# Kernel optimization log

Measured on AMD Instinct MI355X. Metric: run time of the kernel, lower is better.

The kernel has to match this reference:

```python
import jax, jax.numpy as jnp
import numpy as np

EPS = 1e-5

def _layer_norm_last(x):
    # F.layer_norm over the last dim, no affine
    m = jnp.mean(x, axis=-1, keepdims=True)
    v = jnp.var(x, axis=-1, keepdims=True)
    return (x - m) * jax.lax.rsqrt(v + EPS)

def setup_inputs() -> dict:
    key = jax.random.key(0)
    ks = jax.random.split(key, 4)
    N, C, H, W = 8, 512, 32, 32
    G = 8
    x = jax.random.normal(ks[0], (N, C, H, W), dtype=jnp.float32)
    w_qkv = jax.random.normal(ks[1], (3 * C, C), dtype=jnp.float32) * 0.02
    relative = jax.random.normal(ks[2], (3, 2 * C - 1), dtype=jnp.float32)
    bn_w = jnp.ones((3 * G,), dtype=jnp.float32)
    bn_b = jnp.zeros((3 * G,), dtype=jnp.float32)
    return {
        "x": x, "w_qkv": w_qkv, "relative": relative,
        "bn_w": bn_w, "bn_b": bn_b,
        "f_qr": jnp.float32(0.1), "f_kr": jnp.float32(0.1),
        "f_sv": jnp.float32(1.0), "f_sve": jnp.float32(0.1),
        "gamma": jnp.full((1,), 0.5, dtype=jnp.float32),
    }

def reference(x, w_qkv, relative, bn_w, bn_b, f_qr, f_kr, f_sv, f_sve, gamma):
    N, C, H, W = x.shape
    HW = H * W
    G = bn_w.shape[0] // 3          # groups
    gp = HW // G                    # group_planes

    # qkv transform (1x1 conv == matmul over channels) + layernorm over spatial
    x1 = x.reshape(N, C, HW)
    x1 = jnp.einsum('oc,bci->boi', w_qkv, x1)          # (N, 3C, HW)
    x1 = _layer_norm_last(x1)

    qkv = x1.reshape(N, G, 3 * C, gp)                  # row-major, matches torch
    q = qkv[:, :, :C]                                  # (N, G, C, gp)
    k = qkv[:, :, C:2 * C]
    v = qkv[:, :, 2 * C:]

    # relative position embeddings gathered to (3, C, C)
    qi = jnp.arange(C)[None, :]
    ki = jnp.arange(C)[:, None]
    rel_idx = (ki - qi + C - 1).reshape(-1)            # (C*C,) int
    emb = relative[:, rel_idx].reshape(3, C, C)
    qE, kE, vE = emb[0], emb[1], emb[2]

    # 'bgci,icj->bgcj' with emb repeated along i collapses to sum over i then outer
    qr = jnp.einsum('bgci,cj->bgcj', q, qE) * f_qr     # (N, G, C, C)
    kr = jnp.swapaxes(jnp.einsum('bgci,cj->bgcj', k, kE), 2, 3) * f_kr
    qk = jnp.einsum('bgci,bgji->bgcj', q, k)           # (N, G, C, C)

    ss = jnp.concatenate([qk, qr, kr], axis=1)         # (N, 3G, C, C)
    # BatchNorm2d (training mode: batch stats over N, C, C axes)
    mu = jnp.mean(ss, axis=(0, 2, 3), keepdims=True)
    var = jnp.var(ss, axis=(0, 2, 3), keepdims=True)
    ss = (ss - mu) * jax.lax.rsqrt(var + EPS)
    ss = ss * bn_w.reshape(1, -1, 1, 1) + bn_b.reshape(1, -1, 1, 1)

    ss = ss.reshape(N, 3, G, C, C).sum(axis=1)         # (N, G, C, C)
    sim = jax.nn.softmax(ss, axis=3)

    sv = jnp.einsum('bgci,bgij->bgjc', sim, v) * f_sv  # (N, G, gp, C)
    # 'bgci,jci->bgjc' with vE repeated along j -> same value for every j
    sve = jnp.einsum('bgci,ci->bgc', sim, vE) * f_sve  # (N, G, C)
    sve = jnp.broadcast_to(sve[:, :, None, :], sv.shape)

    so = jnp.concatenate([sv, sve], axis=-1).reshape(N, HW * 2, C)
    so = jnp.swapaxes(_layer_norm_last(jnp.swapaxes(so, 1, 2)), 1, 2)
    out = so.reshape(N, G, gp, 2, C).sum(axis=-2).reshape(N, C, H, W)
    return gamma.reshape(()) * out + x
```

## Files before the change

kernel.cpp:

```cpp
#include <hip/hip_runtime.h>
#include <math.h>

#define DEV_INLINE __device__ __forceinline__

typedef short bf16x8 __attribute__((ext_vector_type(8)));
typedef float f32x4  __attribute__((ext_vector_type(4)));


DEV_INLINE float bf2f(short h){
  union { unsigned u; float f; } x; x.u = ((unsigned)(unsigned short)h) << 16; return x.f;
}
DEV_INLINE short f2bf(float f){
  union { float f; unsigned u; } x; x.f = f;
  unsigned r = x.u + 0x7FFF + ((x.u >> 16) & 1);
  return (short)(r >> 16);
}

template<bool MAXOP>
DEV_INLINE float block_reduce_f(float v){
  __shared__ float tmp[4];
  const int lane = threadIdx.x & 63, w = threadIdx.x >> 6;
  #pragma unroll
  for (int off = 32; off; off >>= 1){
    float o = __shfl_down(v, off);
    v = MAXOP ? fmaxf(v, o) : (v + o);
  }
  __syncthreads();
  if (lane == 0) tmp[w] = v;
  __syncthreads();
  return MAXOP ? fmaxf(fmaxf(tmp[0], tmp[1]), fmaxf(tmp[2], tmp[3]))
               : (tmp[0] + tmp[1] + tmp[2] + tmp[3]);
}

DEV_INLINE double block_reduce_d(double v){
  __shared__ double tmp[4];
  const int lane = threadIdx.x & 63, w = threadIdx.x >> 6;
  #pragma unroll
  for (int off = 32; off; off >>= 1) v += __shfl_down(v, off);
  __syncthreads();
  if (lane == 0) tmp[w] = v;
  __syncthreads();
  return tmp[0] + tmp[1] + tmp[2] + tmp[3];
}


DEV_INLINE void stage64(const short* __restrict__ g, int ldk, char* lds_region, int t){
  #pragma unroll
  for (int r = 0; r < 4; ++r){
    int o   = t * 16 + r * 4096;
    int row = o >> 7, wb = o & 127;
    int swb = wb ^ ((row & 7) << 4);
    const short* src = g + (size_t)row * ldk + (swb >> 1);
    char* dst = lds_region + ((t >> 6) << 10) + (r << 12);
    __builtin_amdgcn_global_load_lds((const __attribute__((address_space(1))) void*)src,
                                     (__attribute__((address_space(3))) void*)dst, 16, 0, 0);
  }
}

DEV_INLINE bf16x8 read_frag64(const char* base, int row, int kgrp){
  int off = row * 128 + ((kgrp ^ (row & 7)) << 4);
  return *(const bf16x8*)(base + off);
}

template<int KT64>
DEV_INLINE void mfma_loop64(const short* __restrict__ A, int ldA,
                            const short* __restrict__ B, int ldB,
                            char* ldsA, char* ldsB, int t, f32x4 acc[4][4]){
  const int l = t & 63, w = t >> 6;
  const int wr = (w >> 1) * 64, wc = (w & 1) * 64;
  for (int kt = 0; kt < KT64; ++kt){
    stage64(A + kt * 64, ldA, ldsA, t);
    stage64(B + kt * 64, ldB, ldsB, t);
    __syncthreads();
    #pragma unroll
    for (int h = 0; h < 2; ++h){
      bf16x8 af[4], bfr[4];
      #pragma unroll
      for (int m = 0; m < 4; ++m) af[m]  = read_frag64(ldsA, wr + m * 16 + (l & 15), (l >> 4) + h * 4);
      #pragma unroll
      for (int n = 0; n < 4; ++n) bfr[n] = read_frag64(ldsB, wc + n * 16 + (l & 15), (l >> 4) + h * 4);
      #pragma unroll
      for (int m = 0; m < 4; ++m)
        #pragma unroll
        for (int n = 0; n < 4; ++n)
          acc[m][n] = __builtin_amdgcn_mfma_f32_16x16x32_bf16(af[m], bfr[n], acc[m][n], 0, 0, 0);
    }
    __syncthreads();
  }
}

__global__ __launch_bounds__(256) void k_prep(const float* __restrict__ X, short* __restrict__ Xt,
                                              const float* __restrict__ W, short* __restrict__ Wbf,
                                              double* __restrict__ stats, float* __restrict__ S12){
  __shared__ short s[64][72];
  const int bid = blockIdx.x;
  const int t = threadIdx.x;
  if (bid < 1024){
    const int it = bid & 15, kt = (bid >> 4) & 7, b = bid >> 7;
    const int rl = t >> 2, cs = (t & 3) * 16;
    const float* src = X + ((size_t)b * 512 + kt * 64 + rl) * 1024 + it * 64 + cs;
    #pragma unroll
    for (int e = 0; e < 16; e += 4){
      float4 v = *(const float4*)(src + e);
      s[rl][cs + e + 0] = f2bf(v.x); s[rl][cs + e + 1] = f2bf(v.y);
      s[rl][cs + e + 2] = f2bf(v.z); s[rl][cs + e + 3] = f2bf(v.w);
    }
    __syncthreads();
    bf16x8 a0, a1;
    #pragma unroll
    for (int e = 0; e < 8; ++e){ a0[e] = s[cs + e][rl]; a1[e] = s[cs + 8 + e][rl]; }
    short* dst = Xt + ((size_t)b * 1024 + it * 64 + rl) * 512 + kt * 64 + cs;
    *(bf16x8*)dst = a0;
    *(bf16x8*)(dst + 8) = a1;
  } else {
    const int gi = (bid - 1024) * 256 + t;
    if (gi < 48) stats[gi] = 0.0;
    if (gi < 8192) S12[gi] = 0.f;
    const int i = gi * 4;
    float4 v = *(const float4*)(W + i);
    short4 o; o.x = f2bf(v.x); o.y = f2bf(v.y); o.z = f2bf(v.z); o.w = f2bf(v.w);
    *(short4*)(Wbf + i) = o;
  }
}

__global__ __launch_bounds__(256) void k_gemm1(const short* __restrict__ Wbf,
                                               const short* __restrict__ Xt,
                                               short* __restrict__ Ybf){
  const int b = blockIdx.z, mt = blockIdx.y, nt = blockIdx.x;
  __shared__ char lds[32768];
  const int t = threadIdx.x;
  f32x4 acc[4][4];
  #pragma unroll
  for (int m = 0; m < 4; ++m)
    #pragma unroll
    for (int n = 0; n < 4; ++n) acc[m][n] = {0.f, 0.f, 0.f, 0.f};
  const short* A = Wbf + (size_t)mt * 128 * 512;
  const short* B = Xt + (size_t)b * 1024 * 512 + (size_t)nt * 128 * 512;
  mfma_loop64<8>(A, 512, B, 512, lds, lds + 16384, t, acc);
  const int l = t & 63, w = t >> 6, wr = (w >> 1) * 64, wc = (w & 1) * 64;
  short* out = Ybf + (size_t)b * 1536 * 1024 + (size_t)(mt * 128 + wr) * 1024 + nt * 128 + wc;
  #pragma unroll
  for (int m = 0; m < 4; ++m)
    #pragma unroll
    for (int n = 0; n < 4; ++n)
      #pragma unroll
      for (int j = 0; j < 4; ++j)
        out[(size_t)(m * 16 + (l >> 4) * 4 + j) * 1024 + n * 16 + (l & 15)] = f2bf(acc[m][n][j]);
}

__global__ __launch_bounds__(256) void k_ln(short* __restrict__ Ybf,
                                            float* __restrict__ QS, float* __restrict__ KS){
  const int row = blockIdx.x * 4 + (threadIdx.x >> 6);
  const int l = threadIdx.x & 63;
  short* p = Ybf + (size_t)row * 1024 + l * 16;
  bf16x8 v0 = *(const bf16x8*)p;
  bf16x8 v1 = *(const bf16x8*)(p + 8);
  float f[16];
  #pragma unroll
  for (int e = 0; e < 8; ++e){ f[e] = bf2f(v0[e]); f[8 + e] = bf2f(v1[e]); }
  float s1 = 0.f, s2 = 0.f;
  #pragma unroll
  for (int e = 0; e < 16; ++e){ s1 += f[e]; s2 += f[e] * f[e]; }
  #pragma unroll
  for (int off = 32; off; off >>= 1){ s1 += __shfl_xor(s1, off); s2 += __shfl_xor(s2, off); }
  float mean = s1 * (1.f / 1024.f);
  float r = rsqrtf(s2 * (1.f / 1024.f) - mean * mean + 1e-5f);
  float cs = 0.f;
  #pragma unroll
  for (int e = 0; e < 16; ++e){ f[e] = (f[e] - mean) * r; cs += f[e]; }
  bf16x8 o0, o1;
  #pragma unroll
  for (int e = 0; e < 8; ++e){ o0[e] = f2bf(f[e]); o1[e] = f2bf(f[8 + e]); }
  *(bf16x8*)p = o0;
  *(bf16x8*)(p + 8) = o1;
  cs += __shfl_xor(cs, 1); cs += __shfl_xor(cs, 2); cs += __shfl_xor(cs, 4);
  const int o = row % 1536, ol = o % 192;
  if ((l & 7) == 0 && ol < 128){
    const int b = row / 1536, g = o / 192;
    const int c = (ol & 63) * 8 + (l >> 3);
    const int idx = (b * 8 + g) * 512 + c;
    if (ol < 64) QS[idx] = cs; else KS[idx] = cs;
  }
}

__global__ __launch_bounds__(256) void k_mid(const short* __restrict__ Ybf,
                                             short* __restrict__ QKbf,
                                             short* __restrict__ Vt,
                                             const float* __restrict__ QS,
                                             const float* __restrict__ KS,
                                             const float* __restrict__ rel,
                                             double* __restrict__ stats){
  __shared__ char lds[32768];
  const int bid = blockIdx.x;
  const int t = threadIdx.x;

  if (bid < 64){
    const int g = bid & 7, ch = bid >> 3;
    const int c = ch * 64 + (t >> 2), part = t & 3;
    float r1 = 0, r2 = 0, r3 = 0, r4 = 0;
    for (int d = part * 128; d < part * 128 + 128; ++d){
      float v0 = rel[c + d];        r1 += v0; r2 += v0 * v0;
      float v1 = rel[1023 + c + d]; r3 += v1; r4 += v1 * v1;
    }
    #pragma unroll
    for (int off = 1; off < 4; off <<= 1){
      r1 += __shfl_xor(r1, off); r2 += __shfl_xor(r2, off);
      r3 += __shfl_xor(r3, off); r4 += __shfl_xor(r4, off);
    }
    double sq1 = 0, sq2 = 0, sk1 = 0, sk2 = 0;
    if (part == 0){
      float qa = 0, qb = 0, ka = 0, kb = 0;
      for (int b = 0; b < 8; ++b){
        float v = QS[(size_t)(b * 8 + g) * 512 + c]; qa += v; qb += v * v;
        float w = KS[(size_t)(b * 8 + g) * 512 + c]; ka += w; kb += w * w;
      }
      sq1 = (double)r1 * qa; sq2 = (double)r2 * qb;
      sk1 = (double)r3 * ka; sk2 = (double)r4 * kb;
    }
    sq1 = block_reduce_d(sq1);
    sq2 = block_reduce_d(sq2);
    sk1 = block_reduce_d(sk1);
    sk2 = block_reduce_d(sk2);
    if (t == 0){
      atomicAdd(&stats[g * 6 + 2], sq1);
      atomicAdd(&stats[g * 6 + 3], sq2);
      atomicAdd(&stats[g * 6 + 4], sk1);
      atomicAdd(&stats[g * 6 + 5], sk2);
    }
  } else if (bid < 1088){
    const int qb = bid - 64;
    const int nt = qb & 3, mt = (qb >> 2) & 3, bg = qb >> 4;
    const int b = bg >> 3, g = bg & 7;
    f32x4 acc[4][4];
    #pragma unroll
    for (int m = 0; m < 4; ++m)
      #pragma unroll
      for (int n = 0; n < 4; ++n) acc[m][n] = {0.f, 0.f, 0.f, 0.f};
    const short* q  = Ybf + (size_t)(b * 1536 + g * 192) * 1024;
    const short* kp = q + 65536;
    mfma_loop64<2>(q + (size_t)mt * 128 * 128, 128, kp + (size_t)nt * 128 * 128, 128,
                   lds, lds + 16384, t, acc);
    const int l = t & 63, w = t >> 6, wr = (w >> 1) * 64, wc = (w & 1) * 64;
    short* out = QKbf + (size_t)bg * 262144 + (size_t)(mt * 128 + wr) * 512 + nt * 128 + wc;
    float s1 = 0.f, s2 = 0.f;
    #pragma unroll
    for (int m = 0; m < 4; ++m)
      #pragma unroll
      for (int n = 0; n < 4; ++n)
        #pragma unroll
        for (int j = 0; j < 4; ++j){
          float vl = acc[m][n][j];
          s1 += vl; s2 += vl * vl;
          out[(size_t)(m * 16 + (l >> 4) * 4 + j) * 512 + n * 16 + (l & 15)] = f2bf(vl);
        }
    float S1 = block_reduce_f<false>(s1);
    float S2 = block_reduce_f<false>(s2);
    if (t == 0){
      atomicAdd(&stats[g * 6 + 0], (double)S1);
      atomicAdd(&stats[g * 6 + 1], (double)S2);
    }
  } else {
    const int vb = bid - 1088;
    const int jt = vb & 1, iit = (vb >> 1) & 7, bg = vb >> 4;
    const int b = bg >> 3, g = bg & 7;
    short (*s)[72] = (short(*)[72])lds;
    const short* V = Ybf + (size_t)(b * 1536 + g * 192 + 128) * 1024;
    const int rl = t >> 2, cs = (t & 3) * 16;
    const short* src = V + (size_t)(iit * 64 + rl) * 128 + jt * 64 + cs;
    *(bf16x8*)&s[rl][cs]     = *(const bf16x8*)src;
    *(bf16x8*)&s[rl][cs + 8] = *(const bf16x8*)(src + 8);
    __syncthreads();
    bf16x8 a0, a1;
    #pragma unroll
    for (int e = 0; e < 8; ++e){ a0[e] = s[cs + e][rl]; a1[e] = s[cs + 8 + e][rl]; }
    short* dst = Vt + ((size_t)bg * 128 + jt * 64 + rl) * 512 + iit * 64 + cs;
    *(bf16x8*)dst = a0;
    *(bf16x8*)(dst + 8) = a1;
  }
}

__global__ __launch_bounds__(256) void k_softmax(short* __restrict__ QKbf,
    const float* __restrict__ QS, const float* __restrict__ KS,
    const float* __restrict__ rel, const double* __restrict__ stats,
    const float* __restrict__ bnw, const float* __restrict__ bnb,
    const float* __restrict__ fqr, const float* __restrict__ fkr,
    const float* __restrict__ fsve, float* __restrict__ SVE, float* __restrict__ S12){
  const int row = blockIdx.x * 4 + (threadIdx.x >> 6);
  const int l = threadIdx.x & 63;
  const int bg = row >> 9, c = row & 511, g = bg & 7;
  const double M = 2097152.0;
  double mu0  = stats[g*6+0] / M;
  double var0 = stats[g*6+1] / M - mu0*mu0;
  double A0d  = (double)bnw[g] / sqrt(var0 + 1e-5);
  double fq   = (double)fqr[0];
  double mu1  = fq * stats[g*6+2] / M;
  double var1 = fq*fq * stats[g*6+3] / M - mu1*mu1;
  double A1d  = (double)bnw[8+g] / sqrt(var1 + 1e-5);
  double fk   = (double)fkr[0];
  double mu2  = fk * stats[g*6+4] / M;
  double var2 = fk*fk * stats[g*6+5] / M - mu2*mu2;
  double A2d  = (double)bnw[16+g] / sqrt(var2 + 1e-5);
  double Cgd  = ((double)bnb[g] - mu0*A0d) + ((double)bnb[8+g] - mu1*A1d)
              + ((double)bnb[16+g] - mu2*A2d);
  const float A0 = (float)A0d, B2 = (float)(A2d * fk), Cg = (float)Cgd;
  const float B1q = (float)(A1d * fq) * QS[row];

  short* __restrict__ qkrow = QKbf + (size_t)row * 512;
  const float* __restrict__ ksrow = KS + (size_t)bg * 512;
  const int j0 = l * 8;
  bf16x8 qk8 = *(const bf16x8*)(qkrow + j0);
  float4 ks0 = *(const float4*)(ksrow + j0);
  float4 ks1 = *(const float4*)(ksrow + j0 + 4);
  float ks[8] = {ks0.x, ks0.y, ks0.z, ks0.w, ks1.x, ks1.y, ks1.z, ks1.w};
  const float* relq = rel + 511 + c - j0;
  const float* relk = rel + 1534 + j0 - c;
  float s[8];
  float sum = 0.f;
  #pragma unroll
  for (int e = 0; e < 8; ++e){
    float sc = A0 * bf2f(qk8[e]) + B1q * relq[-e] + B2 * ks[e] * relk[e] + Cg;
    s[e] = __expf(sc);
    sum += s[e];
  }
  #pragma unroll
  for (int off = 32; off; off >>= 1) sum += __shfl_xor(sum, off);
  const float inv = 1.0f / sum;
  const float* relv = rel + 2557 + c - j0;
  float sve = 0.f;
  bf16x8 p8;
  #pragma unroll
  for (int e = 0; e < 8; ++e){
    float p = s[e] * inv;
    p8[e] = f2bf(p);
    sve += p * relv[-e];
  }
  *(bf16x8*)(qkrow + j0) = p8;
  #pragma unroll
  for (int off = 32; off; off >>= 1) sve += __shfl_xor(sve, off);
  if (l == 0){
    float e = fsve[0] * sve;
    SVE[row] = e;
    const int b = bg >> 3;
    atomicAdd(&S12[b * 512 + c],        128.f * e);
    atomicAdd(&S12[4096 + b * 512 + c], 128.f * e * e);
  }
}

__global__ __launch_bounds__(256) void k_sv(const short* __restrict__ Pbf,
                                            const short* __restrict__ Vt,
                                            const float* __restrict__ fsv,
                                            short* __restrict__ SV2,
                                            float* __restrict__ S12){
  const int bg = blockIdx.z, mt = blockIdx.x;
  __shared__ char lds[32768];
  __shared__ float s1buf[128], s2buf[128];
  const int t = threadIdx.x;
  s1buf[t & 127] = 0.f; s2buf[t & 127] = 0.f;
  f32x4 acc[4][4];
  #pragma unroll
  for (int m = 0; m < 4; ++m)
    #pragma unroll
    for (int n = 0; n < 4; ++n) acc[m][n] = {0.f, 0.f, 0.f, 0.f};
  const short* A = Pbf + (size_t)bg * 262144 + (size_t)mt * 128 * 512;
  const short* B = Vt  + (size_t)bg * 65536;
  mfma_loop64<8>(A, 512, B, 512, lds, lds + 16384, t, acc);
  const int l = t & 63, w = t >> 6, wr = (w >> 1) * 64, wc = (w & 1) * 64;
  const float fv = fsv[0];
  short* out = SV2 + (size_t)bg * 65536 + (size_t)(mt * 128 + wr) * 128 + wc;
  #pragma unroll
  for (int m = 0; m < 4; ++m)
    #pragma unroll
    for (int jr = 0; jr < 4; ++jr){
      float p1 = 0.f, p2 = 0.f;
      #pragma unroll
      for (int n = 0; n < 4; ++n){
        float vl = acc[m][n][jr] * fv;
        p1 += vl; p2 += vl * vl;
        out[(size_t)(m * 16 + (l >> 4) * 4 + jr) * 128 + n * 16 + (l & 15)] = f2bf(vl);
      }
      #pragma unroll
      for (int off = 1; off < 16; off <<= 1){
        p1 += __shfl_xor(p1, off);
        p2 += __shfl_xor(p2, off);
      }
      if ((l & 15) == 0){
        int rloc = wr + m * 16 + (l >> 4) * 4 + jr;
        atomicAdd(&s1buf[rloc], p1);
        atomicAdd(&s2buf[rloc], p2);
      }
    }
  __syncthreads();
  if (t < 128){
    const int b = bg >> 3;
    const int ci = b * 512 + mt * 128 + t;
    atomicAdd(&S12[ci],        s1buf[t]);
    atomicAdd(&S12[4096 + ci], s2buf[t]);
  }
}

__global__ __launch_bounds__(256) void k_out(const short* __restrict__ SV2,
    const float* __restrict__ SVE, const float* __restrict__ S12,
    const float* __restrict__ X, const float* __restrict__ gam, float* __restrict__ OUT){
  const int c2t = blockIdx.x, g = blockIdx.y, b = blockIdx.z;
  const int bg = b * 8 + g;
  const int c20 = c2t * 64;
  __shared__ float s[64][129];
  const int t = threadIdx.x;
  {
    const int col8 = (t & 15) * 8;
    #pragma unroll
    for (int r0 = 0; r0 < 64; r0 += 16){
      int row = r0 + (t >> 4);
      bf16x8 v = *(const bf16x8*)(SV2 + (size_t)bg * 65536 + (size_t)(c20 + row) * 128 + col8);
      #pragma unroll
      for (int e = 0; e < 8; ++e) s[row][col8 + e] = bf2f(v[e]);
    }
  }
  __syncthreads();
  const int lane = t & 63, w = t >> 6;
  const int c2 = c20 + lane;
  const float sm1 = S12[b * 512 + c2];
  const float sm2 = S12[4096 + b * 512 + c2];
  const float mean = sm1 * (1.f / 2048.f);
  const float rs   = rsqrtf(sm2 * (1.f / 2048.f) - mean * mean + 1e-5f);
  const float e    = SVE[(size_t)bg * 512 + c2];
  const float gm   = gam[0];
  for (int j = w; j < 128; j += 4){
    float v = s[lane][j];
    float o = (v + e - 2.f * mean) * rs;
    int chan = g * 64 + (j >> 1);
    size_t oi = ((size_t)b * 512 + chan) * 1024 + ((j & 1) << 9) + c2;
    OUT[oi] = gm * o + X[oi];
  }
}

extern "C" void kernel_launch(void* const* d_in, const int* in_sizes, int n_in,
                              void* d_out, int out_size, void* d_ws, size_t ws_size,
                              hipStream_t stream){
  const float* X    = (const float*)d_in[0];
  const float* W    = (const float*)d_in[1];
  const float* REL  = (const float*)d_in[2];
  const float* BNW  = (const float*)d_in[3];
  const float* BNB  = (const float*)d_in[4];
  const float* FQR  = (const float*)d_in[5];
  const float* FKR  = (const float*)d_in[6];
  const float* FSV  = (const float*)d_in[7];
  const float* FSVE = (const float*)d_in[8];
  const float* GAM  = (const float*)d_in[9];
  float* OUT = (float*)d_out;

  char* ws = (char*)d_ws;
  short*  Ybf   = (short*) (ws + 0ull);
  short*  QKbf  = (short*) (ws + 25165824ull);
  short*  SV2   = (short*) (ws + 58720256ull);
  short*  Wbf   = (short*) (ws + 75497472ull);
  short*  Xt    = (short*) (ws + 77070336ull);
  short*  Vt    = (short*) (ws + 85458944ull);
  float*  QS    = (float*) (ws + 93847552ull);
  float*  KS    = (float*) (ws + 93978624ull);
  float*  SVE   = (float*) (ws + 94109696ull);
  double* STATS = (double*)(ws + 94240768ull);
  float*  S12   = (float*) (ws + 94249472ull);

  k_prep   <<<1792,            256, 0, stream>>>(X, Xt, W, Wbf, STATS, S12);
  k_gemm1  <<<dim3(8, 12, 8),  256, 0, stream>>>(Wbf, Xt, Ybf);
  k_ln     <<<3072,            256, 0, stream>>>(Ybf, QS, KS);
  k_mid    <<<2112,            256, 0, stream>>>(Ybf, QKbf, Vt, QS, KS, REL, STATS);
  k_softmax<<<8192,            256, 0, stream>>>(QKbf, QS, KS, REL, STATS,
                                                 BNW, BNB, FQR, FKR, FSVE, SVE, S12);
  k_sv     <<<dim3(4, 1, 64),  256, 0, stream>>>(QKbf, Vt, FSV, SV2, S12);
  k_out    <<<dim3(8, 8, 8),   256, 0, stream>>>(SV2, SVE, S12, X, GAM, OUT);
}
```

Measured before the change: 114.2 us.

## Fuse softmax with sim@V matmul, keeping probabilities in LDS

Merges the softmax kernel and the sim×V MFMA kernel into one kernel. Each block computes unnormalized exponentials for 32 rows into swizzled LDS, then runs the MFMA against staged V tiles and applies 1/sum at the epilogue. This drops the bf16 probability write-back and its re-read from global memory, plus one launch. The cost is a smaller M tile (32 rows), which gives less reuse of V per block, and V is re-streamed by 16 blocks per group.

```diff
diff --git a/kernel.cpp b/kernel.cpp
--- a/kernel.cpp
+++ b/kernel.cpp
@@ -279,15 +279,22 @@
   }
 }
 
-__global__ __launch_bounds__(256) void k_softmax(short* __restrict__ QKbf,
+__global__ __launch_bounds__(256) void k_smsv(const short* __restrict__ QKbf,
+    const short* __restrict__ Vt,
     const float* __restrict__ QS, const float* __restrict__ KS,
     const float* __restrict__ rel, const double* __restrict__ stats,
     const float* __restrict__ bnw, const float* __restrict__ bnb,
     const float* __restrict__ fqr, const float* __restrict__ fkr,
-    const float* __restrict__ fsve, float* __restrict__ SVE, float* __restrict__ S12){
-  const int row = blockIdx.x * 4 + (threadIdx.x >> 6);
-  const int l = threadIdx.x & 63;
-  const int bg = row >> 9, c = row & 511, g = bg & 7;
+    const float* __restrict__ fsv, const float* __restrict__ fsve,
+    float* __restrict__ SVE, short* __restrict__ SV2, float* __restrict__ S12){
+  const int mt = blockIdx.x, bg = blockIdx.y;
+  const int b = bg >> 3, g = bg & 7;
+  __shared__ char Plds[32768];
+  __shared__ char Vlds[16384];
+  __shared__ float rowinv[32];
+  __shared__ float s1buf[32], s2buf[32];
+  const int t = threadIdx.x;
+
   const double M = 2097152.0;
   double mu0  = stats[g*6+0] / M;
   double var0 = stats[g*6+1] / M - mu0*mu0;
@@ -303,96 +310,102 @@
   double Cgd  = ((double)bnb[g] - mu0*A0d) + ((double)bnb[8+g] - mu1*A1d)
               + ((double)bnb[16+g] - mu2*A2d);
   const float A0 = (float)A0d, B2 = (float)(A2d * fk), Cg = (float)Cgd;
-  const float B1q = (float)(A1d * fq) * QS[row];
-
-  short* __restrict__ qkrow = QKbf + (size_t)row * 512;
-  const float* __restrict__ ksrow = KS + (size_t)bg * 512;
-  const int j0 = l * 8;
-  bf16x8 qk8 = *(const bf16x8*)(qkrow + j0);
-  float4 ks0 = *(const float4*)(ksrow + j0);
-  float4 ks1 = *(const float4*)(ksrow + j0 + 4);
-  float ks[8] = {ks0.x, ks0.y, ks0.z, ks0.w, ks1.x, ks1.y, ks1.z, ks1.w};
-  const float* relq = rel + 511 + c - j0;
-  const float* relk = rel + 1534 + j0 - c;
-  float s[8];
-  float sum = 0.f;
-  #pragma unroll
-  for (int e = 0; e < 8; ++e){
-    float sc = A0 * bf2f(qk8[e]) + B1q * relq[-e] + B2 * ks[e] * relk[e] + Cg;
-    s[e] = __expf(sc);
-    sum += s[e];
-  }
-  #pragma unroll
-  for (int off = 32; off; off >>= 1) sum += __shfl_xor(sum, off);
-  const float inv = 1.0f / sum;
-  const float* relv = rel + 2557 + c - j0;
-  float sve = 0.f;
-  bf16x8 p8;
-  #pragma unroll
-  for (int e = 0; e < 8; ++e){
-    float p = s[e] * inv;
-    p8[e] = f2bf(p);
-    sve += p * relv[-e];
-  }
-  *(bf16x8*)(qkrow + j0) = p8;
-  #pragma unroll
-  for (int off = 32; off; off >>= 1) sve += __shfl_xor(sve, off);
-  if (l == 0){
-    float e = fsve[0] * sve;
-    SVE[row] = e;
-    const int b = bg >> 3;
-    atomicAdd(&S12[b * 512 + c],        128.f * e);
-    atomicAdd(&S12[4096 + b * 512 + c], 128.f * e * e);
-  }
-}
-
-__global__ __launch_bounds__(256) void k_sv(const short* __restrict__ Pbf,
-                                            const short* __restrict__ Vt,
-                                            const float* __restrict__ fsv,
-                                            short* __restrict__ SV2,
-                                            float* __restrict__ S12){
-  const int bg = blockIdx.z, mt = blockIdx.x;
-  __shared__ char lds[32768];
-  __shared__ float s1buf[128], s2buf[128];
-  const int t = threadIdx.x;
-  s1buf[t & 127] = 0.f; s2buf[t & 127] = 0.f;
-  f32x4 acc[4][4];
-  #pragma unroll
-  for (int m = 0; m < 4; ++m)
-    #pragma unroll
-    for (int n = 0; n < 4; ++n) acc[m][n] = {0.f, 0.f, 0.f, 0.f};
-  const short* A = Pbf + (size_t)bg * 262144 + (size_t)mt * 128 * 512;
-  const short* B = Vt  + (size_t)bg * 65536;
-  mfma_loop64<8>(A, 512, B, 512, lds, lds + 16384, t, acc);
-  const int l = t & 63, w = t >> 6, wr = (w >> 1) * 64, wc = (w & 1) * 64;
+  const float B1f = (float)(A1d * fq);
+
+  {
+    const int r = t >> 3, q = t & 7;
+    const int c = mt * 32 + r;
+    const int grow = bg * 512 + c;
+    const float B1q = B1f * QS[grow];
+    const short* __restrict__ qkrow = QKbf + (size_t)bg * 262144 + (size_t)c * 512;
+    const float* __restrict__ ksrow = KS + (size_t)bg * 512;
+    const float* relq = rel + 511 + c;
+    const float* relk = rel + 1534 - c;
+    const float* relv = rel + 2557 + c;
+    float sum = 0.f, svea = 0.f;
+    #pragma unroll
+    for (int u = 0; u < 8; ++u){
+      const int j0 = q * 64 + u * 8;
+      bf16x8 qk8 = *(const bf16x8*)(qkrow + j0);
+      float4 k0 = *(const float4*)(ksrow + j0);
+      float4 k1 = *(const float4*)(ksrow + j0 + 4);
+      float ks[8] = {k0.x, k0.y, k0.z, k0.w, k1.x, k1.y, k1.z, k1.w};
+      bf16x8 p8;
+      #pragma unroll
+      for (int e = 0; e < 8; ++e){
+        const int j = j0 + e;
+        float sc = A0 * bf2f(qk8[e]) + B1q * relq[-j] + B2 * ks[e] * relk[j] + Cg;
+        float es = __expf(sc);
+        sum  += es;
+        svea += es * relv[-j];
+        p8[e] = f2bf(es);
+      }
+      *(bf16x8*)(Plds + r * 1024 + ((j0 * 2) ^ ((r & 7) << 4))) = p8;
+    }
+    sum  += __shfl_xor(sum, 1);  sum  += __shfl_xor(sum, 2);  sum  += __shfl_xor(sum, 4);
+    svea += __shfl_xor(svea, 1); svea += __shfl_xor(svea, 2); svea += __shfl_xor(svea, 4);
+    const float inv = 1.0f / sum;
+    if (q == 0){
+      rowinv[r] = inv;
+      float e = fsve[0] * svea * inv;
+      SVE[grow] = e;
+      atomicAdd(&S12[b * 512 + c],        128.f * e);
+      atomicAdd(&S12[4096 + b * 512 + c], 128.f * e * e);
+    }
+  }
+  if (t < 32){ s1buf[t] = 0.f; s2buf[t] = 0.f; }
+  __syncthreads();
+
+  const int l = t & 63, w = t >> 6;
+  const int wr = (w >> 1) * 16, wc = (w & 1) * 64;
+  f32x4 acc[4];
+  #pragma unroll
+  for (int n = 0; n < 4; ++n) acc[n] = {0.f, 0.f, 0.f, 0.f};
+  const int arow = wr + (l & 15);
+  for (int kt = 0; kt < 8; ++kt){
+    stage64(Vt + (size_t)bg * 65536 + kt * 64, 512, Vlds, t);
+    __syncthreads();
+    #pragma unroll
+    for (int h = 0; h < 2; ++h){
+      const int slot = kt * 8 + (l >> 4) + h * 4;
+      bf16x8 af = *(const bf16x8*)(Plds + arow * 1024 + ((slot ^ (arow & 7)) << 4));
+      bf16x8 bfr[4];
+      #pragma unroll
+      for (int n = 0; n < 4; ++n)
+        bfr[n] = read_frag64(Vlds, wc + n * 16 + (l & 15), (l >> 4) + h * 4);
+      #pragma unroll
+      for (int n = 0; n < 4; ++n)
+        acc[n] = __builtin_amdgcn_mfma_f32_16x16x32_bf16(af, bfr[n], acc[n], 0, 0, 0);
+    }
+    __syncthreads();
+  }
+
   const float fv = fsv[0];
-  short* out = SV2 + (size_t)bg * 65536 + (size_t)(mt * 128 + wr) * 128 + wc;
-  #pragma unroll
-  for (int m = 0; m < 4; ++m)
-    #pragma unroll
-    for (int jr = 0; jr < 4; ++jr){
-      float p1 = 0.f, p2 = 0.f;
-      #pragma unroll
-      for (int n = 0; n < 4; ++n){
-        float vl = acc[m][n][jr] * fv;
-        p1 += vl; p2 += vl * vl;
-        out[(size_t)(m * 16 + (l >> 4) * 4 + jr) * 128 + n * 16 + (l & 15)] = f2bf(vl);
-      }
-      #pragma unroll
-      for (int off = 1; off < 16; off <<= 1){
-        p1 += __shfl_xor(p1, off);
-        p2 += __shfl_xor(p2, off);
-      }
-      if ((l & 15) == 0){
-        int rloc = wr + m * 16 + (l >> 4) * 4 + jr;
-        atomicAdd(&s1buf[rloc], p1);
-        atomicAdd(&s2buf[rloc], p2);
-      }
-    }
-  __syncthreads();
-  if (t < 128){
-    const int b = bg >> 3;
-    const int ci = b * 512 + mt * 128 + t;
+  short* out = SV2 + (size_t)bg * 65536 + (size_t)(mt * 32 + wr) * 128 + wc;
+  #pragma unroll
+  for (int jr = 0; jr < 4; ++jr){
+    const int rloc = wr + (l >> 4) * 4 + jr;
+    const float sc = rowinv[rloc] * fv;
+    float p1 = 0.f, p2 = 0.f;
+    #pragma unroll
+    for (int n = 0; n < 4; ++n){
+      float vl = acc[n][jr] * sc;
+      p1 += vl; p2 += vl * vl;
+      out[(size_t)((l >> 4) * 4 + jr) * 128 + n * 16 + (l & 15)] = f2bf(vl);
+    }
+    #pragma unroll
+    for (int off = 1; off < 16; off <<= 1){
+      p1 += __shfl_xor(p1, off);
+      p2 += __shfl_xor(p2, off);
+    }
+    if ((l & 15) == 0){
+      atomicAdd(&s1buf[rloc], p1);
+      atomicAdd(&s2buf[rloc], p2);
+    }
+  }
+  __syncthreads();
+  if (t < 32){
+    const int ci = b * 512 + mt * 32 + t;
     atomicAdd(&S12[ci],        s1buf[t]);
     atomicAdd(&S12[4096 + ci], s2buf[t]);
   }
@@ -462,12 +475,12 @@
   double* STATS = (double*)(ws + 94240768ull);
   float*  S12   = (float*) (ws + 94249472ull);
 
-  k_prep   <<<1792,            256, 0, stream>>>(X, Xt, W, Wbf, STATS, S12);
-  k_gemm1  <<<dim3(8, 12, 8),  256, 0, stream>>>(Wbf, Xt, Ybf);
-  k_ln     <<<3072,            256, 0, stream>>>(Ybf, QS, KS);
-  k_mid    <<<2112,            256, 0, stream>>>(Ybf, QKbf, Vt, QS, KS, REL, STATS);
-  k_softmax<<<8192,            256, 0, stream>>>(QKbf, QS, KS, REL, STATS,
-                                                 BNW, BNB, FQR, FKR, FSVE, SVE, S12);
-  k_sv     <<<dim3(4, 1, 64),  256, 0, stream>>>(QKbf, Vt, FSV, SV2, S12);
-  k_out    <<<dim3(8, 8, 8),   256, 0, stream>>>(SV2, SVE, S12, X, GAM, OUT);
-}
+  k_prep <<<1792,            256, 0, stream>>>(X, Xt, W, Wbf, STATS, S12);
+  k_gemm1<<<dim3(8, 12, 8),  256, 0, stream>>>(Wbf, Xt, Ybf);
+  k_ln   <<<3072,            256, 0, stream>>>(Ybf, QS, KS);
+  k_mid  <<<2112,            256, 0, stream>>>(Ybf, QKbf, Vt, QS, KS, REL, STATS);
+  k_smsv <<<dim3(16, 64),    256, 0, stream>>>(QKbf, Vt, QS, KS, REL, STATS,
+                                               BNW, BNB, FQR, FKR, FSV, FSVE,
+                                               SVE, SV2, S12);
+  k_out  <<<dim3(8, 8, 8),   256, 0, stream>>>(SV2, SVE, S12, X, GAM, OUT);
+}
```

New measurement: 117.0 us. +2.5%, slower.
